# Kernel tuning notes

Measured on AMD Instinct MI355X. Metric: run time of the kernel, lower is better.

## Reference

```python
import jax, jax.numpy as jnp
import numpy as np

N, C, D = 8192, 6, 512


def setup_inputs() -> dict:
    key = jax.random.key(0)
    k1, k2, k3, k4 = jax.random.split(key, 4)
    logits = jax.random.normal(k1, (N, C), dtype=jnp.float32)      # unused by the loss
    targets = jax.random.uniform(k2, (N, C), dtype=jnp.float32)    # soft labels
    features = jax.random.normal(k3, (N, D), dtype=jnp.float32)
    weights = jax.random.uniform(k4, (N,), dtype=jnp.float32)
    t = jnp.asarray(10.0, dtype=jnp.float32)   # nn.Parameter init
    b = jnp.asarray(-10.0, dtype=jnp.float32)  # nn.Parameter init
    return {"logits": logits, "targets": targets, "features": features,
            "weights": weights, "t": t, "b": b}


def reference(logits, targets, features, weights, t, b):
    # F.normalize(features, p=2, dim=1) with eps=1e-12 clamp like torch
    norm = jnp.maximum(jnp.linalg.norm(features, axis=1, keepdims=True), 1e-12)
    f = features / norm                                   # [N, D]
    sim = jnp.einsum('nd,md->nm', f, f)                   # [N, N] cosine similarity
    agree = 2.0 * jnp.einsum('nc,mc->nm', targets, targets) - 1.0  # [N, N]
    elements = agree * (t * sim + b)
    # -log(1/(1+exp(e))) == softplus(e) == -log_sigmoid(-e), numerically stable
    loss = (1.0 / N) * (-jax.nn.log_sigmoid(-elements)).sum(axis=1)  # [N]
    loss = loss * weights / weights.mean()
    return loss
```

## Files before the change

### kernel.cpp

```cpp
#include <hip/hip_runtime.h>
#include <hip/hip_bf16.h>


#define NROW 8192
#define DIM  512
#define NCLS 6

#define BM 128
#define BK 64
#define NB (NROW / BM)
#define NTRI (NB * (NB + 1) / 2)
#define NSTG 8

typedef short s16x8 __attribute__((ext_vector_type(8)));
typedef float f32x4 __attribute__((ext_vector_type(4)));

static __device__ __forceinline__ ushort f2bf(float x) {
    __hip_bfloat16 h = __float2bfloat16(x);
    union { __hip_bfloat16 h; ushort u; } c; c.h = h; return c.u;
}
static __device__ __forceinline__ float bf2f(ushort u) {
    union { __hip_bfloat16 h; ushort u; } c; c.u = u; return __bfloat162float(c.h);
}

__global__ __launch_bounds__(256) void k_prep(const float* __restrict__ feat,
                                              const float* __restrict__ tgt,
                                              const float* __restrict__ w,
                                              ushort* __restrict__ fpack,
                                              ushort* __restrict__ tpA,
                                              ushort* __restrict__ tpB,
                                              float* __restrict__ partial,
                                              float* __restrict__ wsum) {
    const int wave = threadIdx.x >> 6, lane = threadIdx.x & 63;
    const int row = blockIdx.x * 4 + wave;
    const float* fr = feat + (size_t)row * DIM;
    float4 v0 = *(const float4*)(fr + lane * 4);
    float4 v1 = *(const float4*)(fr + 256 + lane * 4);
    float ss = v0.x*v0.x + v0.y*v0.y + v0.z*v0.z + v0.w*v0.w
             + v1.x*v1.x + v1.y*v1.y + v1.z*v1.z + v1.w*v1.w;
#pragma unroll
    for (int m = 1; m < 64; m <<= 1) ss += __shfl_xor(ss, m);
    const float inv = 1.f / fmaxf(sqrtf(ss), 1e-12f);

    float vals[8] = {v0.x, v0.y, v0.z, v0.w, v1.x, v1.y, v1.z, v1.w};
    ushort hi[8];
#pragma unroll
    for (int i = 0; i < 8; ++i) hi[i] = f2bf(vals[i] * inv);
    ushort* dst = fpack + (size_t)row * 512;
    *(ushort4*)(dst + lane * 4)       = make_ushort4(hi[0], hi[1], hi[2], hi[3]);
    *(ushort4*)(dst + 256 + lane * 4) = make_ushort4(hi[4], hi[5], hi[6], hi[7]);

    if (lane < 32) {
        float ta = 0.f, tb = 0.f;
        if (lane < 18) {
            int c = (lane < 6) ? lane : (lane < 12 ? lane - 6 : lane - 12);
            float x = tgt[(size_t)row * NCLS + c];
            ushort h = f2bf(x);
            float hf = bf2f(h);
            float l = x - hf;
            if (lane < 6)       { ta = hf; tb = hf; }
            else if (lane < 12) { ta = l;  tb = hf; }
            else                { ta = hf; tb = l;  }
        }
        tpA[(size_t)row * 32 + lane] = f2bf(ta);
        tpB[(size_t)row * 32 + lane] = f2bf(tb);
    }

    __shared__ float red[4];
    if (lane == 0) {
        partial[row] = 0.f;
        red[wave] = w[row];
    }
    __syncthreads();
    if (threadIdx.x == 0)
        atomicAdd(wsum, red[0] + red[1] + red[2] + red[3]);
}

__device__ __forceinline__ void stage_f(const ushort* __restrict__ src,
                                        ushort* lds, int tid) {
#pragma unroll
    for (int i = 0; i < 4; ++i) {
        int q = i * 256 + tid;
        int r = q >> 3, c = q & 7;
        __builtin_amdgcn_global_load_lds(
            (const __attribute__((address_space(1))) void*)(src + (size_t)r * 512 + c * 8),
            (__attribute__((address_space(3))) void*)(lds + q * 8),
            16, 0, 0);
    }
}
__device__ __forceinline__ void stage_t(const ushort* __restrict__ src,
                                        ushort* lds, int tid) {
#pragma unroll
    for (int i = 0; i < 2; ++i) {
        int q = i * 256 + tid;
        int r = q >> 2, c = q & 3;
        __builtin_amdgcn_global_load_lds(
            (const __attribute__((address_space(1))) void*)(src + (size_t)r * 32 + c * 8),
            (__attribute__((address_space(3))) void*)(lds + q * 8),
            16, 0, 0);
    }
}

__global__ __launch_bounds__(256, 3) void k_gemm(
    const ushort* __restrict__ fpack, const ushort* __restrict__ tpA,
    const ushort* __restrict__ tpB, const float* __restrict__ tp,
    const float* __restrict__ bp, float* __restrict__ partial) {

    const int orig = blockIdx.x;
    const int b = (orig & 7) * (NTRI / 8) + (orig >> 3);
    int bi = 0, rem = b;
    while (rem >= NB - bi) { rem -= NB - bi; ++bi; }
    const int bj = bi + rem;

    __shared__ ushort sA[BM * BK];
    __shared__ ushort sB[BM * BK];

    const int tid = threadIdx.x;
    const int lane = tid & 63;
    const int wave = tid >> 6;
    const int wr = wave >> 1, wc = wave & 1;

    const float tt = *tp, bb = *bp;

    f32x4 accS[4][4], accT[4][4];
#pragma unroll
    for (int i = 0; i < 4; ++i)
#pragma unroll
        for (int j = 0; j < 4; ++j) {
            accS[i][j] = (f32x4){0.f, 0.f, 0.f, 0.f};
            accT[i][j] = (f32x4){0.f, 0.f, 0.f, 0.f};
        }

    const ushort* baseA = fpack + (size_t)(bi * BM) * 512;
    const ushort* baseB = fpack + (size_t)(bj * BM) * 512;

    for (int s = 0; s < NSTG; ++s) {
        stage_f(baseA + s * 64, &sA[0], tid);
        stage_f(baseB + s * 64, &sB[0], tid);
        __syncthreads();
#pragma unroll
        for (int kk = 0; kk < 2; ++kk) {
            s16x8 af[4], bg[4];
            const int kb = kk * 32 + (lane >> 4) * 8;
            const int rr = lane & 15;
#pragma unroll
            for (int i = 0; i < 4; ++i)
                af[i] = *(const s16x8*)(&sA[(wr * 64 + i * 16 + rr) * BK + kb]);
#pragma unroll
            for (int j = 0; j < 4; ++j)
                bg[j] = *(const s16x8*)(&sB[(wc * 64 + j * 16 + rr) * BK + kb]);
#pragma unroll
            for (int i = 0; i < 4; ++i)
#pragma unroll
                for (int j = 0; j < 4; ++j)
                    accS[i][j] = __builtin_amdgcn_mfma_f32_16x16x32_bf16(
                        af[i], bg[j], accS[i][j], 0, 0, 0);
        }
        __syncthreads();
    }

    stage_t(tpA + (size_t)(bi * BM) * 32, &sA[0], tid);
    stage_t(tpB + (size_t)(bj * BM) * 32, &sB[0], tid);
    __syncthreads();
    {
        s16x8 af[4], bg[4];
        const int kb = (lane >> 4) * 8;
        const int rr = lane & 15;
#pragma unroll
        for (int i = 0; i < 4; ++i)
            af[i] = *(const s16x8*)(&sA[(wr * 64 + i * 16 + rr) * 32 + kb]);
#pragma unroll
        for (int j = 0; j < 4; ++j)
            bg[j] = *(const s16x8*)(&sB[(wc * 64 + j * 16 + rr) * 32 + kb]);
#pragma unroll
        for (int i = 0; i < 4; ++i)
#pragma unroll
            for (int j = 0; j < 4; ++j)
                accT[i][j] = __builtin_amdgcn_mfma_f32_16x16x32_bf16(
                    af[i], bg[j], accT[i][j], 0, 0, 0);
    }

    float rowsum[4][4];
    float colsum[4];
#pragma unroll
    for (int i = 0; i < 4; ++i)
#pragma unroll
        for (int r = 0; r < 4; ++r) rowsum[i][r] = 0.f;
#pragma unroll
    for (int j = 0; j < 4; ++j) colsum[j] = 0.f;

#pragma unroll
    for (int i = 0; i < 4; ++i)
#pragma unroll
        for (int j = 0; j < 4; ++j)
#pragma unroll
            for (int r = 0; r < 4; ++r) {
                const float agree = fmaf(2.f, accT[i][j][r], -1.f);
                const float e = agree * fmaf(tt, accS[i][j][r], bb);
                const float sp = fmaxf(e, 0.f) + __logf(1.f + __expf(-fabsf(e)));
                rowsum[i][r] += sp;
                colsum[j] += sp;
            }

#pragma unroll
    for (int i = 0; i < 4; ++i)
#pragma unroll
        for (int r = 0; r < 4; ++r) {
            float v = rowsum[i][r];
            v += __shfl_xor(v, 1); v += __shfl_xor(v, 2);
            v += __shfl_xor(v, 4); v += __shfl_xor(v, 8);
            if ((lane & 15) == 0)
                atomicAdd(&partial[bi * BM + wr * 64 + i * 16 + (lane >> 4) * 4 + r], v);
        }
    if (bi != bj) {
#pragma unroll
        for (int j = 0; j < 4; ++j) {
            float v = colsum[j];
            v += __shfl_xor(v, 16); v += __shfl_xor(v, 32);
            if (lane < 16)
                atomicAdd(&partial[bj * BM + wc * 64 + j * 16 + lane], v);
        }
    }
}

__global__ __launch_bounds__(256) void k_final(const float* __restrict__ partial,
                                               const float* __restrict__ w,
                                               const float* __restrict__ wsum,
                                               float* __restrict__ out) {
    int i = blockIdx.x * 256 + threadIdx.x;
    out[i] = partial[i] * w[i] / wsum[0];
}

extern "C" void kernel_launch(void* const* d_in, const int* in_sizes, int n_in,
                              void* d_out, int out_size, void* d_ws, size_t ws_size,
                              hipStream_t stream) {
    const float* targets  = (const float*)d_in[1];
    const float* features = (const float*)d_in[2];
    const float* weights  = (const float*)d_in[3];
    const float* tp       = (const float*)d_in[4];
    const float* bp       = (const float*)d_in[5];
    float* out = (float*)d_out;

    char* p = (char*)d_ws;
    ushort* fpack   = (ushort*)p; p += (size_t)NROW * 512 * sizeof(ushort);
    ushort* tpA     = (ushort*)p; p += (size_t)NROW * 32 * sizeof(ushort);
    ushort* tpB     = (ushort*)p; p += (size_t)NROW * 32 * sizeof(ushort);
    float*  partial = (float*)p;  p += (size_t)NROW * sizeof(float);
    float*  wsum    = (float*)p;

    hipMemsetAsync(wsum, 0, sizeof(float), stream);
    k_prep<<<NROW / 4, 256, 0, stream>>>(features, targets, weights, fpack, tpA, tpB,
                                         partial, wsum);
    k_gemm<<<NTRI, 256, 0, stream>>>(fpack, tpA, tpB, tp, bp, partial);
    k_final<<<NROW / 256, 256, 0, stream>>>(partial, weights, wsum, out);
}
```

Baseline: 185.9 us.

## Double-buffer LDS staging in GEMM and drop memset/atomic weight sum

New measurement: 191.3 us. 2.9% more time.

```diff
diff --git a/kernel.cpp b/kernel.cpp
--- a/kernel.cpp
+++ b/kernel.cpp
@@ -30,7 +30,7 @@
                                               ushort* __restrict__ tpA,
                                               ushort* __restrict__ tpB,
                                               float* __restrict__ partial,
-                                              float* __restrict__ wsum) {
+                                              float* __restrict__ wpart) {
     const int wave = threadIdx.x >> 6, lane = threadIdx.x & 63;
     const int row = blockIdx.x * 4 + wave;
     const float* fr = feat + (size_t)row * DIM;
@@ -73,7 +73,7 @@
     }
     __syncthreads();
     if (threadIdx.x == 0)
-        atomicAdd(wsum, red[0] + red[1] + red[2] + red[3]);
+        wpart[blockIdx.x] = red[0] + red[1] + red[2] + red[3];
 }
 
 __device__ __forceinline__ void stage_f(const ushort* __restrict__ src,
@@ -101,7 +101,7 @@
     }
 }
 
-__global__ __launch_bounds__(256, 3) void k_gemm(
+__global__ __launch_bounds__(256, 2) void k_gemm(
     const ushort* __restrict__ fpack, const ushort* __restrict__ tpA,
     const ushort* __restrict__ tpB, const float* __restrict__ tp,
     const float* __restrict__ bp, float* __restrict__ partial) {
@@ -112,8 +112,8 @@
     while (rem >= NB - bi) { rem -= NB - bi; ++bi; }
     const int bj = bi + rem;
 
-    __shared__ ushort sA[BM * BK];
-    __shared__ ushort sB[BM * BK];
+    __shared__ ushort sA[2][BM * BK];
+    __shared__ ushort sB[2][BM * BK];
 
     const int tid = threadIdx.x;
     const int lane = tid & 63;
@@ -134,10 +134,19 @@
     const ushort* baseA = fpack + (size_t)(bi * BM) * 512;
     const ushort* baseB = fpack + (size_t)(bj * BM) * 512;
 
+    stage_f(baseA, &sA[0][0], tid);
+    stage_f(baseB, &sB[0][0], tid);
+    __syncthreads();
+
+    int buf = 0;
     for (int s = 0; s < NSTG; ++s) {
-        stage_f(baseA + s * 64, &sA[0], tid);
-        stage_f(baseB + s * 64, &sB[0], tid);
-        __syncthreads();
+        if (s + 1 < NSTG) {
+            stage_f(baseA + (s + 1) * 64, &sA[buf ^ 1][0], tid);
+            stage_f(baseB + (s + 1) * 64, &sB[buf ^ 1][0], tid);
+        } else {
+            stage_t(tpA + (size_t)(bi * BM) * 32, &sA[buf ^ 1][0], tid);
+            stage_t(tpB + (size_t)(bj * BM) * 32, &sB[buf ^ 1][0], tid);
+        }
 #pragma unroll
         for (int kk = 0; kk < 2; ++kk) {
             s16x8 af[4], bg[4];
@@ -145,10 +154,10 @@
             const int rr = lane & 15;
 #pragma unroll
             for (int i = 0; i < 4; ++i)
-                af[i] = *(const s16x8*)(&sA[(wr * 64 + i * 16 + rr) * BK + kb]);
+                af[i] = *(const s16x8*)(&sA[buf][(wr * 64 + i * 16 + rr) * BK + kb]);
 #pragma unroll
             for (int j = 0; j < 4; ++j)
-                bg[j] = *(const s16x8*)(&sB[(wc * 64 + j * 16 + rr) * BK + kb]);
+                bg[j] = *(const s16x8*)(&sB[buf][(wc * 64 + j * 16 + rr) * BK + kb]);
 #pragma unroll
             for (int i = 0; i < 4; ++i)
 #pragma unroll
@@ -157,21 +166,19 @@
                         af[i], bg[j], accS[i][j], 0, 0, 0);
         }
         __syncthreads();
-    }
-
-    stage_t(tpA + (size_t)(bi * BM) * 32, &sA[0], tid);
-    stage_t(tpB + (size_t)(bj * BM) * 32, &sB[0], tid);
-    __syncthreads();
+        buf ^= 1;
+    }
+
     {
         s16x8 af[4], bg[4];
         const int kb = (lane >> 4) * 8;
         const int rr = lane & 15;
 #pragma unroll
         for (int i = 0; i < 4; ++i)
-            af[i] = *(const s16x8*)(&sA[(wr * 64 + i * 16 + rr) * 32 + kb]);
+            af[i] = *(const s16x8*)(&sA[buf][(wr * 64 + i * 16 + rr) * 32 + kb]);
 #pragma unroll
         for (int j = 0; j < 4; ++j)
-            bg[j] = *(const s16x8*)(&sB[(wc * 64 + j * 16 + rr) * 32 + kb]);
+            bg[j] = *(const s16x8*)(&sB[buf][(wc * 64 + j * 16 + rr) * 32 + kb]);
 #pragma unroll
         for (int i = 0; i < 4; ++i)
 #pragma unroll
@@ -225,10 +232,18 @@
 
 __global__ __launch_bounds__(256) void k_final(const float* __restrict__ partial,
                                                const float* __restrict__ w,
-                                               const float* __restrict__ wsum,
+                                               const float* __restrict__ wpart,
                                                float* __restrict__ out) {
+    __shared__ float red[4];
+    float s = 0.f;
+    for (int i = threadIdx.x; i < NROW / 4; i += 256) s += wpart[i];
+#pragma unroll
+    for (int m = 1; m < 64; m <<= 1) s += __shfl_xor(s, m);
+    if ((threadIdx.x & 63) == 0) red[threadIdx.x >> 6] = s;
+    __syncthreads();
+    const float wsum = red[0] + red[1] + red[2] + red[3];
     int i = blockIdx.x * 256 + threadIdx.x;
-    out[i] = partial[i] * w[i] / wsum[0];
+    out[i] = partial[i] * w[i] / wsum;
 }
 
 extern "C" void kernel_launch(void* const* d_in, const int* in_sizes, int n_in,
@@ -246,11 +261,10 @@
     ushort* tpA     = (ushort*)p; p += (size_t)NROW * 32 * sizeof(ushort);
     ushort* tpB     = (ushort*)p; p += (size_t)NROW * 32 * sizeof(ushort);
     float*  partial = (float*)p;  p += (size_t)NROW * sizeof(float);
-    float*  wsum    = (float*)p;
-
-    hipMemsetAsync(wsum, 0, sizeof(float), stream);
+    float*  wpart   = (float*)p;  p += (size_t)(NROW / 4) * sizeof(float);
+
     k_prep<<<NROW / 4, 256, 0, stream>>>(features, targets, weights, fpack, tpA, tpB,
-                                         partial, wsum);
+                                         partial, wpart);
     k_gemm<<<NTRI, 256, 0, stream>>>(fpack, tpA, tpB, tp, bp, partial);
-    k_final<<<NROW / 256, 256, 0, stream>>>(partial, weights, wsum, out);
-}
+    k_final<<<NROW / 256, 256, 0, stream>>>(partial, weights, wpart, out);
+}
```

## Fuse final normalization into GEMM via last-block counter, widen K tile

Applied to the files above, without the earlier changes.

Result: slower. 313.9 us (+68.8%).

```diff
diff --git a/kernel.cpp b/kernel.cpp
--- a/kernel.cpp
+++ b/kernel.cpp
@@ -7,10 +7,10 @@
 #define NCLS 6
 
 #define BM 128
-#define BK 64
+#define BK 128
 #define NB (NROW / BM)
 #define NTRI (NB * (NB + 1) / 2)
-#define NSTG 8
+#define NSTG 4
 
 typedef short s16x8 __attribute__((ext_vector_type(8)));
 typedef float f32x4 __attribute__((ext_vector_type(4)));
@@ -30,7 +30,8 @@
                                               ushort* __restrict__ tpA,
                                               ushort* __restrict__ tpB,
                                               float* __restrict__ partial,
-                                              float* __restrict__ wsum) {
+                                              float* __restrict__ wpart,
+                                              unsigned* __restrict__ counter) {
     const int wave = threadIdx.x >> 6, lane = threadIdx.x & 63;
     const int row = blockIdx.x * 4 + wave;
     const float* fr = feat + (size_t)row * DIM;
@@ -72,16 +73,18 @@
         red[wave] = w[row];
     }
     __syncthreads();
-    if (threadIdx.x == 0)
-        atomicAdd(wsum, red[0] + red[1] + red[2] + red[3]);
+    if (threadIdx.x == 0) {
+        wpart[blockIdx.x] = red[0] + red[1] + red[2] + red[3];
+        if (blockIdx.x == 0) *counter = 0u;
+    }
 }
 
 __device__ __forceinline__ void stage_f(const ushort* __restrict__ src,
                                         ushort* lds, int tid) {
 #pragma unroll
-    for (int i = 0; i < 4; ++i) {
+    for (int i = 0; i < 8; ++i) {
         int q = i * 256 + tid;
-        int r = q >> 3, c = q & 7;
+        int r = q >> 4, c = q & 15;
         __builtin_amdgcn_global_load_lds(
             (const __attribute__((address_space(1))) void*)(src + (size_t)r * 512 + c * 8),
             (__attribute__((address_space(3))) void*)(lds + q * 8),
@@ -101,10 +104,12 @@
     }
 }
 
-__global__ __launch_bounds__(256, 3) void k_gemm(
+__global__ __launch_bounds__(256, 2) void k_gemm(
     const ushort* __restrict__ fpack, const ushort* __restrict__ tpA,
     const ushort* __restrict__ tpB, const float* __restrict__ tp,
-    const float* __restrict__ bp, float* __restrict__ partial) {
+    const float* __restrict__ bp, const float* __restrict__ w,
+    float* __restrict__ partial, float* __restrict__ wpart,
+    unsigned* __restrict__ counter, float* __restrict__ out) {
 
     const int orig = blockIdx.x;
     const int b = (orig & 7) * (NTRI / 8) + (orig >> 3);
@@ -135,11 +140,11 @@
     const ushort* baseB = fpack + (size_t)(bj * BM) * 512;
 
     for (int s = 0; s < NSTG; ++s) {
-        stage_f(baseA + s * 64, &sA[0], tid);
-        stage_f(baseB + s * 64, &sB[0], tid);
+        stage_f(baseA + s * BK, &sA[0], tid);
+        stage_f(baseB + s * BK, &sB[0], tid);
         __syncthreads();
 #pragma unroll
-        for (int kk = 0; kk < 2; ++kk) {
+        for (int kk = 0; kk < 4; ++kk) {
             s16x8 af[4], bg[4];
             const int kb = kk * 32 + (lane >> 4) * 8;
             const int rr = lane & 15;
@@ -221,14 +226,24 @@
                 atomicAdd(&partial[bj * BM + wc * 64 + j * 16 + lane], v);
         }
     }
-}
-
-__global__ __launch_bounds__(256) void k_final(const float* __restrict__ partial,
-                                               const float* __restrict__ w,
-                                               const float* __restrict__ wsum,
-                                               float* __restrict__ out) {
-    int i = blockIdx.x * 256 + threadIdx.x;
-    out[i] = partial[i] * w[i] / wsum[0];
+
+    __threadfence();
+    __shared__ bool sLast;
+    if (tid == 0)
+        sLast = (atomicAdd(counter, 1u) == NTRI - 1);
+    __syncthreads();
+    if (sLast) {
+        __shared__ float red[4];
+        float s = 0.f;
+        for (int i = tid; i < NROW / 4; i += 256) s += wpart[i];
+#pragma unroll
+        for (int m = 1; m < 64; m <<= 1) s += __shfl_xor(s, m);
+        if ((tid & 63) == 0) red[tid >> 6] = s;
+        __syncthreads();
+        const float wsum = red[0] + red[1] + red[2] + red[3];
+        for (int i = tid; i < NROW; i += 256)
+            out[i] = atomicAdd(&partial[i], 0.f) * w[i] / wsum;
+    }
 }
 
 extern "C" void kernel_launch(void* const* d_in, const int* in_sizes, int n_in,
@@ -242,15 +257,15 @@
     float* out = (float*)d_out;
 
     char* p = (char*)d_ws;
-    ushort* fpack   = (ushort*)p; p += (size_t)NROW * 512 * sizeof(ushort);
-    ushort* tpA     = (ushort*)p; p += (size_t)NROW * 32 * sizeof(ushort);
-    ushort* tpB     = (ushort*)p; p += (size_t)NROW * 32 * sizeof(ushort);
-    float*  partial = (float*)p;  p += (size_t)NROW * sizeof(float);
-    float*  wsum    = (float*)p;
-
-    hipMemsetAsync(wsum, 0, sizeof(float), stream);
+    ushort*   fpack   = (ushort*)p;   p += (size_t)NROW * 512 * sizeof(ushort);
+    ushort*   tpA     = (ushort*)p;   p += (size_t)NROW * 32 * sizeof(ushort);
+    ushort*   tpB     = (ushort*)p;   p += (size_t)NROW * 32 * sizeof(ushort);
+    float*    partial = (float*)p;    p += (size_t)NROW * sizeof(float);
+    float*    wpart   = (float*)p;    p += (size_t)(NROW / 4) * sizeof(float);
+    unsigned* counter = (unsigned*)p;
+
     k_prep<<<NROW / 4, 256, 0, stream>>>(features, targets, weights, fpack, tpA, tpB,
-                                         partial, wsum);
-    k_gemm<<<NTRI, 256, 0, stream>>>(fpack, tpA, tpB, tp, bp, partial);
-    k_final<<<NROW / 256, 256, 0, stream>>>(partial, weights, wsum, out);
-}
+                                         partial, wpart, counter);
+    k_gemm<<<NTRI, 256, 0, stream>>>(fpack, tpA, tpB, tp, bp, weights,
+                                     partial, wpart, counter, out);
+}
```
